# Optimization experiments

Measured on AMD Instinct MI355X. Metric: run time of the kernel, lower is better.

## Reference

```python
import jax, jax.numpy as jnp
import numpy as np

DIM = 64        # feature size per vector
CODES = 512     # codebook size (called d_model in the torch module)
DECAY = 0.99
EPS = 1e-5


def setup_inputs() -> dict:
    key = jax.random.key(0)
    k1, k2 = jax.random.split(key)
    x = jax.random.normal(k1, (64, 64, 64, 64), dtype=jnp.float32)
    embedding = jax.random.normal(k2, (DIM, CODES), dtype=jnp.float32)
    N = jnp.zeros((CODES,), dtype=jnp.float32)
    M = embedding.copy()  # torch module initializes M as embedding.clone()
    return {"x": x, "embedding": embedding, "N": N, "M": M}


def reference(x, embedding, N, M):
    # flatten tokens: [T, DIM]
    flatten = x.reshape(-1, DIM)
    # squared L2 distance to every code: [T, CODES]
    distance = (jnp.sum(flatten * flatten, axis=1, keepdims=True)
                - 2.0 * flatten @ embedding
                + jnp.sum(embedding * embedding, axis=0, keepdims=True))
    max_index = jnp.argmin(distance, axis=1)          # (-distance).max(1) == argmin
    indices = max_index.reshape(x.shape[:-1])
    # gather codes: embedding.T is [CODES, DIM]
    quantize = jnp.take(embedding.T, max_index, axis=0).reshape(x.shape)

    # EMA codebook update (training=True). Avoid materializing onehot:
    # ni = onehot.sum(0); eofx = flatten.T @ onehot  -> segment sums over codes.
    ni = jax.ops.segment_sum(jnp.ones_like(max_index, dtype=jnp.float32),
                             max_index, num_segments=CODES)          # [CODES]
    eofx = jax.ops.segment_sum(flatten, max_index, num_segments=CODES).T  # [DIM, CODES]
    N_new = N * DECAY + (1.0 - DECAY) * ni
    M_new = M * DECAY + (1.0 - DECAY) * eofx
    n = jnp.sum(N_new)
    N_smoothed = (N_new + EPS) / (n + CODES * EPS) * n
    embedding_new = M_new / N_smoothed

    quant_loss = jnp.mean((jax.lax.stop_gradient(x) - quantize) ** 2)
    commitment_loss = jnp.mean((jax.lax.stop_gradient(quantize) - x) ** 2)
    quantize_st = x + jax.lax.stop_gradient(quantize - x)  # straight-through
    return (quantize_st, quant_loss, indices, commitment_loss,
            embedding_new, N_new, M_new)
```

## Files before the change

### kernel.cpp

```cpp
#include <hip/hip_runtime.h>
#include <hip/hip_bf16.h>
#include <math.h>

#define DIM 64
#define CODES 512
#define TOKENS 262144
#define XELEMS 16777216

#define DECAYF 0.99f
#define OMDECAY 0.01f
#define EPSF 1e-5f

#define WS_CNORM 0
#define WS_NI    512
#define WS_EOFX  1024
#define WS_LOSS  33792
#define WS_ET    33808
#define WS_IMG   66576
#define WS_PART  99344
#define PART_STRIDE 33280
#define NPART 512

#define OFF_Q    0
#define OFF_QL   16777216
#define OFF_IDX  16777217
#define OFF_CL   17039361
#define OFF_ENEW 17039362
#define OFF_NNEW 17072130
#define OFF_MNEW 17072642

typedef __attribute__((ext_vector_type(8))) short bf16x8;
typedef __attribute__((ext_vector_type(4))) float f32x4;

static __device__ inline void split_bf(float v, short& hi, short& lo) {
  unsigned int b = __float_as_uint(v);
  unsigned int hb = b & 0xffff0000u;
  float lof = v - __uint_as_float(hb);
  hi = (short)(b >> 16);
  lo = (short)(__float_as_uint(lof) >> 16);
}

__global__ __launch_bounds__(256) void vq_prep(const float* __restrict__ emb,
                                               float* __restrict__ ws) {
  int c = blockIdx.x * 256 + threadIdx.x;
  unsigned short* img = (unsigned short*)(ws + WS_IMG);
  float* eT = ws + WS_ET;
  int cc = c >> 4;
  int n = c & 15;
  float cn = 0.f;
#pragma unroll
  for (int d0 = 0; d0 < DIM; d0 += 4) {
    float v[4];
#pragma unroll
    for (int u = 0; u < 4; ++u) {
      v[u] = emb[(d0 + u) * CODES + c];
      cn = fmaf(v[u], v[u], cn);
    }
    *(float4*)(eT + (size_t)c * DIM + d0) = make_float4(v[0], v[1], v[2], v[3]);
    int kh = d0 >> 5, kk = d0 & 31, qd = kk >> 3, j0 = kk & 7;
    int lane = qd * 16 + n;
    short hi[4], lo[4];
#pragma unroll
    for (int u = 0; u < 4; ++u) split_bf(v[u], hi[u], lo[u]);
    int base = cc * 2048 + kh * 1024 + lane * 8 + j0;
    *(ushort4*)(img + base) =
        make_ushort4((unsigned short)hi[0], (unsigned short)hi[1],
                     (unsigned short)hi[2], (unsigned short)hi[3]);
    *(ushort4*)(img + base + 512) =
        make_ushort4((unsigned short)lo[0], (unsigned short)lo[1],
                     (unsigned short)lo[2], (unsigned short)lo[3]);
  }
  ws[WS_CNORM + c] = cn;
}

__global__ __launch_bounds__(512, 4) void vq_fused(
    const float* __restrict__ x, const float* __restrict__ ws,
    float* __restrict__ loss_sum, float* __restrict__ q_out,
    float* __restrict__ idx_out, float* __restrict__ part_base, int aflush,
    float* __restrict__ ws_acc) {
  __shared__ __align__(16) unsigned char smem[71808];
  float* lds_e = (float*)smem;
  float* lds_n = (float*)(smem + 65664);
  float* cn_l = (float*)(smem + 67712);
  int* win_l = (int*)(smem + 69760);

  const float* eT = ws + WS_ET;
  const unsigned short* gimg = (const unsigned short*)(ws + WS_IMG);

  {
    float4 z = make_float4(0.f, 0.f, 0.f, 0.f);
    float4* zp = (float4*)smem;
    for (int i = threadIdx.x; i < 67712 / 16; i += 512) zp[i] = z;
    for (int i = threadIdx.x; i < CODES; i += 512) cn_l[i] = ws[WS_CNORM + i];
  }
  __syncthreads();

  const int lane = threadIdx.x & 63;
  const int wave = threadIdx.x >> 6;
  const int n = lane & 15;
  const int quad = lane >> 4;
  const int t0 = blockIdx.x * 512 + wave * 64;

  const float INITP = __uint_as_float((__float_as_uint(1e30f) & 0xFFFFFE00u) | 511u);
  float loss = 0.f;

#pragma unroll 1
  for (int pair = 0; pair < 2; ++pair) {
    bf16x8 ah[2][2], al[2][2];
#pragma unroll
    for (int tile = 0; tile < 2; ++tile) {
      const float* xr =
          x + (size_t)(t0 + (pair * 2 + tile) * 16 + n) * DIM + quad * 8;
#pragma unroll
      for (int kh = 0; kh < 2; ++kh) {
        float4 va = *(const float4*)(xr + kh * 32);
        float4 vb = *(const float4*)(xr + kh * 32 + 4);
        float f[8] = {va.x, va.y, va.z, va.w, vb.x, vb.y, vb.z, vb.w};
#pragma unroll
        for (int j = 0; j < 8; ++j) {
          short hi, lo;
          split_bf(-2.f * f[j], hi, lo);
          ah[tile][kh][j] = hi;
          al[tile][kh][j] = lo;
        }
      }
    }

    float v1[2][4], v2[2][4];
#pragma unroll
    for (int tile = 0; tile < 2; ++tile)
#pragma unroll
      for (int r = 0; r < 4; ++r) {
        v1[tile][r] = INITP;
        v2[tile][r] = INITP;
      }

    bf16x8 Pa0, Pa1, Pa2, Pa3, Pb0, Pb1, Pb2, Pb3;
    {
      const unsigned short* bq = gimg + lane * 8;
      Pa0 = *(const bf16x8*)(bq);
      Pa1 = *(const bf16x8*)(bq + 512);
      Pa2 = *(const bf16x8*)(bq + 1024);
      Pa3 = *(const bf16x8*)(bq + 1536);
    }

    auto ccbody = [&](int cc, const bf16x8& ch0, const bf16x8& cl0,
                      const bf16x8& ch1, const bf16x8& cl1, bf16x8& nh0,
                      bf16x8& nl0, bf16x8& nh1, bf16x8& nl1) {
      const unsigned short* bq = gimg + ((cc + 1) & 31) * 2048 + lane * 8;
      nh0 = *(const bf16x8*)(bq);
      nl0 = *(const bf16x8*)(bq + 512);
      nh1 = *(const bf16x8*)(bq + 1024);
      nl1 = *(const bf16x8*)(bq + 1536);
      float cnv = cn_l[cc * 16 + n];
      unsigned int cid = (unsigned int)(cc * 16 + n);
#pragma unroll
      for (int tile = 0; tile < 2; ++tile) {
        f32x4 acc = {0.f, 0.f, 0.f, 0.f};
        acc = __builtin_amdgcn_mfma_f32_16x16x32_bf16(ah[tile][0], ch0, acc, 0, 0, 0);
        acc = __builtin_amdgcn_mfma_f32_16x16x32_bf16(al[tile][0], ch0, acc, 0, 0, 0);
        acc = __builtin_amdgcn_mfma_f32_16x16x32_bf16(ah[tile][0], cl0, acc, 0, 0, 0);
        acc = __builtin_amdgcn_mfma_f32_16x16x32_bf16(ah[tile][1], ch1, acc, 0, 0, 0);
        acc = __builtin_amdgcn_mfma_f32_16x16x32_bf16(al[tile][1], ch1, acc, 0, 0, 0);
        acc = __builtin_amdgcn_mfma_f32_16x16x32_bf16(ah[tile][1], cl1, acc, 0, 0, 0);
#pragma unroll
        for (int r = 0; r < 4; ++r) {
          float s = acc[r] + cnv;
          float sp = __uint_as_float((__float_as_uint(s) & 0xFFFFFE00u) | cid);
          float o1 = v1[tile][r];
          v2[tile][r] = __builtin_amdgcn_fmed3f(sp, o1, v2[tile][r]);
          v1[tile][r] = fminf(sp, o1);
        }
      }
    };

    for (int cc = 0; cc < 32; cc += 2) {
      ccbody(cc, Pa0, Pa1, Pa2, Pa3, Pb0, Pb1, Pb2, Pb3);
      ccbody(cc + 1, Pb0, Pb1, Pb2, Pb3, Pa0, Pa1, Pa2, Pa3);
    }

#pragma unroll
    for (int m = 1; m < 16; m <<= 1) {
#pragma unroll
      for (int tile = 0; tile < 2; ++tile)
#pragma unroll
        for (int r = 0; r < 4; ++r) {
          float o1 = __shfl_xor(v1[tile][r], m, 16);
          float o2 = __shfl_xor(v2[tile][r], m, 16);
          float a = v1[tile][r];
          v1[tile][r] = fminf(a, o1);
          v2[tile][r] = fminf(fminf(v2[tile][r], o2), fmaxf(a, o1));
        }
    }

#pragma unroll
    for (int tile = 0; tile < 2; ++tile) {
      int tt = pair * 2 + tile;
#pragma unroll
      for (int r = 0; r < 4; ++r) {
        int t = t0 + tt * 16 + quad * 4 + r;
        int c1 = (int)(__float_as_uint(v1[tile][r]) & 511u);
        int c2 = (int)(__float_as_uint(v2[tile][r]) & 511u);
        float4 xv = *(const float4*)(x + (size_t)t * DIM + n * 4);
        float4 e1 = *(const float4*)(eT + (size_t)c1 * DIM + n * 4);
        float4 e2 = *(const float4*)(eT + (size_t)c2 * DIM + n * 4);
        float p1 = xv.x * e1.x;
        p1 = fmaf(xv.y, e1.y, p1);
        p1 = fmaf(xv.z, e1.z, p1);
        p1 = fmaf(xv.w, e1.w, p1);
        float p2 = xv.x * e2.x;
        p2 = fmaf(xv.y, e2.y, p2);
        p2 = fmaf(xv.z, e2.z, p2);
        p2 = fmaf(xv.w, e2.w, p2);
#pragma unroll
        for (int m = 1; m < 16; m <<= 1) {
          p1 += __shfl_xor(p1, m, 16);
          p2 += __shfl_xor(p2, m, 16);
        }
        float d1 = fmaf(-2.f, p1, cn_l[c1]);
        float d2 = fmaf(-2.f, p2, cn_l[c2]);
        bool take2 = (d2 < d1) || (d2 == d1 && c2 < c1);
        int w = take2 ? c2 : c1;
        float4 q = take2 ? e2 : e1;
        *(float4*)(q_out + (size_t)t * DIM + n * 4) = q;
        float u0 = xv.x - q.x, u1 = xv.y - q.y;
        float u2 = xv.z - q.z, u3 = xv.w - q.w;
        loss = fmaf(u0, u0, loss);
        loss = fmaf(u1, u1, loss);
        loss = fmaf(u2, u2, loss);
        loss = fmaf(u3, u3, loss);
        if (n == 0) {
          idx_out[t] = (float)w;
          win_l[wave * 64 + tt * 16 + quad * 4 + r] = w;
        }
      }
    }
  }

#pragma unroll
  for (int off = 32; off > 0; off >>= 1) loss += __shfl_down(loss, off, 64);
  if (lane == 0) atomicAdd(loss_sum, loss);

  __syncthreads();

#pragma unroll 1
  for (int kh = 0; kh < 2; ++kh) {
#pragma unroll
    for (int tile = 0; tile < 4; ++tile) {
      int wbi = win_l[wave * 64 + tile * 16 + n];
      if (kh == 0 && quad == 0) atomicAdd(&lds_n[wbi], 1.0f);
      const float* xr =
          x + (size_t)(t0 + tile * 16 + n) * DIM + kh * 32 + quad * 8;
      float4 xa = *(const float4*)(xr);
      float4 xb = *(const float4*)(xr + 4);
      int k0 = quad * 8;
      atomicAdd(&lds_e[(k0 + 0) * 513 + wbi], xa.x);
      atomicAdd(&lds_e[(k0 + 1) * 513 + wbi], xa.y);
      atomicAdd(&lds_e[(k0 + 2) * 513 + wbi], xa.z);
      atomicAdd(&lds_e[(k0 + 3) * 513 + wbi], xa.w);
      atomicAdd(&lds_e[(k0 + 4) * 513 + wbi], xb.x);
      atomicAdd(&lds_e[(k0 + 5) * 513 + wbi], xb.y);
      atomicAdd(&lds_e[(k0 + 6) * 513 + wbi], xb.z);
      atomicAdd(&lds_e[(k0 + 7) * 513 + wbi], xb.w);
    }
    __syncthreads();
    if (aflush) {
      if (kh == 0) {
        for (int i = threadIdx.x; i < CODES; i += 512) {
          float v = lds_n[i];
          if (v != 0.f) atomicAdd(&ws_acc[WS_NI + i], v);
        }
      }
      for (int i = threadIdx.x; i < 32 * CODES; i += 512) {
        int k = i >> 9, c = i & 511;
        float v = lds_e[k * 513 + c];
        if (v != 0.f) atomicAdd(&ws_acc[WS_EOFX + kh * 32 * CODES + i], v);
        if (kh == 0) lds_e[k * 513 + c] = 0.f;
      }
    } else {
      float* dest = part_base + (size_t)blockIdx.x * PART_STRIDE;
      if (kh == 0) {
        for (int i = threadIdx.x; i < CODES; i += 512) dest[i] = lds_n[i];
      }
      for (int i = threadIdx.x; i < 32 * CODES; i += 512) {
        int k = i >> 9, c = i & 511;
        dest[CODES + kh * 32 * CODES + i] = lds_e[k * 513 + c];
        if (kh == 0) lds_e[k * 513 + c] = 0.f;
      }
    }
    if (kh == 0) __syncthreads();
  }
}

__global__ __launch_bounds__(256) void vq_reduce(const float* __restrict__ part,
                                                 float* __restrict__ ws, int P) {
  int i = blockIdx.x * 256 + threadIdx.x;
  if (i >= PART_STRIDE) return;
  float a0 = 0.f, a1 = 0.f, a2 = 0.f, a3 = 0.f;
  int p = 0;
  for (; p + 3 < P; p += 4) {
    a0 += part[(size_t)(p + 0) * PART_STRIDE + i];
    a1 += part[(size_t)(p + 1) * PART_STRIDE + i];
    a2 += part[(size_t)(p + 2) * PART_STRIDE + i];
    a3 += part[(size_t)(p + 3) * PART_STRIDE + i];
  }
  for (; p < P; ++p) a0 += part[(size_t)p * PART_STRIDE + i];
  ws[WS_NI + i] = (a0 + a1) + (a2 + a3);
}

__global__ __launch_bounds__(512) void vq_final(const float* __restrict__ Nin,
                                                const float* __restrict__ Min,
                                                const float* __restrict__ ws,
                                                float* __restrict__ out) {
  __shared__ float red[512];
  int c = threadIdx.x;
  int d = blockIdx.x;
  float niv = ws[WS_NI + c];
  float Nn = Nin[c] * DECAYF + OMDECAY * niv;
  red[c] = Nn;
  __syncthreads();
#pragma unroll
  for (int s = 256; s > 0; s >>= 1) {
    if (c < s) red[c] += red[c + s];
    __syncthreads();
  }
  float nsum = red[0];
  float Nsm = (Nn + EPSF) / (nsum + (float)CODES * EPSF) * nsum;
  float m = Min[d * CODES + c] * DECAYF + OMDECAY * ws[WS_EOFX + d * CODES + c];
  out[OFF_MNEW + d * CODES + c] = m;
  out[OFF_ENEW + d * CODES + c] = m / Nsm;
  if (d == 0) {
    out[OFF_NNEW + c] = Nn;
    if (c == 0) {
      float l = ws[WS_LOSS] / (float)XELEMS;
      out[OFF_QL] = l;
      out[OFF_CL] = l;
    }
  }
}

extern "C" void kernel_launch(void* const* d_in, const int* in_sizes, int n_in,
                              void* d_out, int out_size, void* d_ws, size_t ws_size,
                              hipStream_t stream) {
  const float* x = (const float*)d_in[0];
  const float* emb = (const float*)d_in[1];
  const float* Nin = (const float*)d_in[2];
  const float* Min = (const float*)d_in[3];
  float* out = (float*)d_out;
  float* ws = (float*)d_ws;

  size_t avail = ws_size / 4;
  int aflush = (avail < (size_t)WS_PART + (size_t)NPART * PART_STRIDE) ? 1 : 0;

  hipMemsetAsync(ws + WS_NI, 0, (size_t)(WS_ET - WS_NI) * sizeof(float), stream);

  vq_prep<<<2, 256, 0, stream>>>(emb, ws);

  vq_fused<<<TOKENS / 512, 512, 0, stream>>>(
      x, ws, ws + WS_LOSS, out + OFF_Q, out + OFF_IDX, ws + WS_PART, aflush, ws);

  if (!aflush) {
    vq_reduce<<<(PART_STRIDE + 255) / 256, 256, 0, stream>>>(ws + WS_PART, ws,
                                                             NPART);
  }

  vq_final<<<DIM, 512, 0, stream>>>(Nin, Min, ws, out);
}
```

Before: 350.2 us.

## Stage codebook tiles through LDS with async triple buffering; split reduce across partitions

Codebook image chunks are no longer loaded per wave straight from global memory into registers. Wave 0 now streams them into a triple-buffered LDS ring with global_load_lds, gated by explicit vmcnt waits and workgroup barriers, so the other waves read them from LDS. This cuts redundant global and L2 traffic for the code images, at the cost of one barrier per code chunk. The LDS zeroing moves after the distance loop because the ring reuses that memory, and vq_reduce is split over 8 partition groups that combine results with atomic adds to expose more parallelism.

New measurement: 311.6 us. 1.12x faster.

```diff
diff --git a/kernel.cpp b/kernel.cpp
--- a/kernel.cpp
+++ b/kernel.cpp
@@ -31,6 +31,11 @@
 
 typedef __attribute__((ext_vector_type(8))) short bf16x8;
 typedef __attribute__((ext_vector_type(4))) float f32x4;
+
+#define GLOAD_LDS16(gp, lp)                                        \
+  __builtin_amdgcn_global_load_lds(                                \
+      (const __attribute__((address_space(1))) void*)(gp),         \
+      (__attribute__((address_space(3))) void*)(lp), 16, 0, 0)
 
 static __device__ inline void split_bf(float v, short& hi, short& lo) {
   unsigned int b = __float_as_uint(v);
@@ -85,15 +90,9 @@
   int* win_l = (int*)(smem + 69760);
 
   const float* eT = ws + WS_ET;
-  const unsigned short* gimg = (const unsigned short*)(ws + WS_IMG);
-
-  {
-    float4 z = make_float4(0.f, 0.f, 0.f, 0.f);
-    float4* zp = (float4*)smem;
-    for (int i = threadIdx.x; i < 67712 / 16; i += 512) zp[i] = z;
-    for (int i = threadIdx.x; i < CODES; i += 512) cn_l[i] = ws[WS_CNORM + i];
-  }
-  __syncthreads();
+  const char* gib = (const char*)(ws + WS_IMG);
+
+  for (int i = threadIdx.x; i < CODES; i += 512) cn_l[i] = ws[WS_CNORM + i];
 
   const int lane = threadIdx.x & 63;
   const int wave = threadIdx.x >> 6;
@@ -135,34 +134,41 @@
         v2[tile][r] = INITP;
       }
 
-    bf16x8 Pa0, Pa1, Pa2, Pa3, Pb0, Pb1, Pb2, Pb3;
-    {
-      const unsigned short* bq = gimg + lane * 8;
-      Pa0 = *(const bf16x8*)(bq);
-      Pa1 = *(const bf16x8*)(bq + 512);
-      Pa2 = *(const bf16x8*)(bq + 1024);
-      Pa3 = *(const bf16x8*)(bq + 1536);
-    }
-
-    auto ccbody = [&](int cc, const bf16x8& ch0, const bf16x8& cl0,
-                      const bf16x8& ch1, const bf16x8& cl1, bf16x8& nh0,
-                      bf16x8& nl0, bf16x8& nh1, bf16x8& nl1) {
-      const unsigned short* bq = gimg + ((cc + 1) & 31) * 2048 + lane * 8;
-      nh0 = *(const bf16x8*)(bq);
-      nl0 = *(const bf16x8*)(bq + 512);
-      nh1 = *(const bf16x8*)(bq + 1024);
-      nl1 = *(const bf16x8*)(bq + 1536);
+    if (wave == 0) {
+#pragma unroll
+      for (int c0 = 0; c0 < 2; ++c0)
+#pragma unroll
+        for (int q = 0; q < 4; ++q)
+          GLOAD_LDS16(gib + c0 * 4096 + q * 1024 + (size_t)lane * 16,
+                      (char*)smem + c0 * 4096 + q * 1024);
+    }
+    __syncthreads();
+
+#pragma unroll 1
+    for (int cc = 0; cc < 32; ++cc) {
+      const unsigned short* bp =
+          (const unsigned short*)((const char*)smem + (cc % 3) * 4096);
+      bf16x8 bh0 = *(const bf16x8*)(bp + lane * 8);
+      bf16x8 bl0 = *(const bf16x8*)(bp + 512 + lane * 8);
+      bf16x8 bh1 = *(const bf16x8*)(bp + 1024 + lane * 8);
+      bf16x8 bl1 = *(const bf16x8*)(bp + 1536 + lane * 8);
+      if (wave == 0 && cc < 30) {
+        char* lb = (char*)smem + ((cc + 2) % 3) * 4096;
+        const char* gs = gib + (cc + 2) * 4096 + (size_t)lane * 16;
+#pragma unroll
+        for (int q = 0; q < 4; ++q) GLOAD_LDS16(gs + q * 1024, lb + q * 1024);
+      }
       float cnv = cn_l[cc * 16 + n];
       unsigned int cid = (unsigned int)(cc * 16 + n);
 #pragma unroll
       for (int tile = 0; tile < 2; ++tile) {
         f32x4 acc = {0.f, 0.f, 0.f, 0.f};
-        acc = __builtin_amdgcn_mfma_f32_16x16x32_bf16(ah[tile][0], ch0, acc, 0, 0, 0);
-        acc = __builtin_amdgcn_mfma_f32_16x16x32_bf16(al[tile][0], ch0, acc, 0, 0, 0);
-        acc = __builtin_amdgcn_mfma_f32_16x16x32_bf16(ah[tile][0], cl0, acc, 0, 0, 0);
-        acc = __builtin_amdgcn_mfma_f32_16x16x32_bf16(ah[tile][1], ch1, acc, 0, 0, 0);
-        acc = __builtin_amdgcn_mfma_f32_16x16x32_bf16(al[tile][1], ch1, acc, 0, 0, 0);
-        acc = __builtin_amdgcn_mfma_f32_16x16x32_bf16(ah[tile][1], cl1, acc, 0, 0, 0);
+        acc = __builtin_amdgcn_mfma_f32_16x16x32_bf16(ah[tile][0], bh0, acc, 0, 0, 0);
+        acc = __builtin_amdgcn_mfma_f32_16x16x32_bf16(al[tile][0], bh0, acc, 0, 0, 0);
+        acc = __builtin_amdgcn_mfma_f32_16x16x32_bf16(ah[tile][0], bl0, acc, 0, 0, 0);
+        acc = __builtin_amdgcn_mfma_f32_16x16x32_bf16(ah[tile][1], bh1, acc, 0, 0, 0);
+        acc = __builtin_amdgcn_mfma_f32_16x16x32_bf16(al[tile][1], bh1, acc, 0, 0, 0);
+        acc = __builtin_amdgcn_mfma_f32_16x16x32_bf16(ah[tile][1], bl1, acc, 0, 0, 0);
 #pragma unroll
         for (int r = 0; r < 4; ++r) {
           float s = acc[r] + cnv;
@@ -172,11 +178,14 @@
           v1[tile][r] = fminf(sp, o1);
         }
       }
-    };
-
-    for (int cc = 0; cc < 32; cc += 2) {
-      ccbody(cc, Pa0, Pa1, Pa2, Pa3, Pb0, Pb1, Pb2, Pb3);
-      ccbody(cc + 1, Pb0, Pb1, Pb2, Pb3, Pa0, Pa1, Pa2, Pa3);
+      if (cc < 30) {
+        asm volatile("s_waitcnt vmcnt(4)" ::: "memory");
+      } else {
+        asm volatile("s_waitcnt vmcnt(0)" ::: "memory");
+      }
+      __builtin_amdgcn_sched_barrier(0);
+      __builtin_amdgcn_s_barrier();
+      __builtin_amdgcn_sched_barrier(0);
     }
 
 #pragma unroll
@@ -241,6 +250,12 @@
   for (int off = 32; off > 0; off >>= 1) loss += __shfl_down(loss, off, 64);
   if (lane == 0) atomicAdd(loss_sum, loss);
 
+  __syncthreads();
+  {
+    float4 z = make_float4(0.f, 0.f, 0.f, 0.f);
+    float4* zp = (float4*)smem;
+    for (int i = threadIdx.x; i < 67712 / 16; i += 512) zp[i] = z;
+  }
   __syncthreads();
 
 #pragma unroll 1
@@ -296,16 +311,19 @@
                                                  float* __restrict__ ws, int P) {
   int i = blockIdx.x * 256 + threadIdx.x;
   if (i >= PART_STRIDE) return;
+  int cp = P >> 3;
+  int p0 = blockIdx.y * cp;
+  int pe = p0 + cp;
   float a0 = 0.f, a1 = 0.f, a2 = 0.f, a3 = 0.f;
-  int p = 0;
-  for (; p + 3 < P; p += 4) {
+  int p = p0;
+  for (; p + 3 < pe; p += 4) {
     a0 += part[(size_t)(p + 0) * PART_STRIDE + i];
     a1 += part[(size_t)(p + 1) * PART_STRIDE + i];
     a2 += part[(size_t)(p + 2) * PART_STRIDE + i];
     a3 += part[(size_t)(p + 3) * PART_STRIDE + i];
   }
-  for (; p < P; ++p) a0 += part[(size_t)p * PART_STRIDE + i];
-  ws[WS_NI + i] = (a0 + a1) + (a2 + a3);
+  for (; p < pe; ++p) a0 += part[(size_t)p * PART_STRIDE + i];
+  atomicAdd(&ws[WS_NI + i], (a0 + a1) + (a2 + a3));
 }
 
 __global__ __launch_bounds__(512) void vq_final(const float* __restrict__ Nin,
@@ -360,8 +378,8 @@
       x, ws, ws + WS_LOSS, out + OFF_Q, out + OFF_IDX, ws + WS_PART, aflush, ws);
 
   if (!aflush) {
-    vq_reduce<<<(PART_STRIDE + 255) / 256, 256, 0, stream>>>(ws + WS_PART, ws,
-                                                             NPART);
+    vq_reduce<<<dim3((PART_STRIDE + 255) / 256, 8), 256, 0, stream>>>(
+        ws + WS_PART, ws, NPART);
   }
 
   vq_final<<<DIM, 512, 0, stream>>>(Nin, Min, ws, out);
```

## Split fused VQ kernel into screening and scatter kernels; parallelize partial reduce

Applied to the files above, without the earlier changes.

Splits the fused distance/argmin and segment-sum kernel into two. The screening kernel uses 256-thread blocks and only a small LDS footprint, which should raise occupancy for the compute-heavy phase. A separate scatter kernel rereads x and the indices to build the per-block partial sums in LDS. The reduce kernel now splits the partials across 8 y-blocks and combines them with atomics, which relies on the NI/EOFX region being zeroed by the memset. The cost is a second full read of x and the indices, plus an extra kernel launch.

After: 327.4 us. 1.07x faster.

```diff
diff --git a/kernel.cpp b/kernel.cpp
--- a/kernel.cpp
+++ b/kernel.cpp
@@ -73,33 +73,23 @@
   ws[WS_CNORM + c] = cn;
 }
 
-__global__ __launch_bounds__(512, 4) void vq_fused(
+__global__ __launch_bounds__(256, 4) void vq_screen(
     const float* __restrict__ x, const float* __restrict__ ws,
     float* __restrict__ loss_sum, float* __restrict__ q_out,
-    float* __restrict__ idx_out, float* __restrict__ part_base, int aflush,
-    float* __restrict__ ws_acc) {
-  __shared__ __align__(16) unsigned char smem[71808];
-  float* lds_e = (float*)smem;
-  float* lds_n = (float*)(smem + 65664);
-  float* cn_l = (float*)(smem + 67712);
-  int* win_l = (int*)(smem + 69760);
+    float* __restrict__ idx_out) {
+  __shared__ float cn_l[CODES];
 
   const float* eT = ws + WS_ET;
   const unsigned short* gimg = (const unsigned short*)(ws + WS_IMG);
 
-  {
-    float4 z = make_float4(0.f, 0.f, 0.f, 0.f);
-    float4* zp = (float4*)smem;
-    for (int i = threadIdx.x; i < 67712 / 16; i += 512) zp[i] = z;
-    for (int i = threadIdx.x; i < CODES; i += 512) cn_l[i] = ws[WS_CNORM + i];
-  }
+  for (int i = threadIdx.x; i < CODES; i += 256) cn_l[i] = ws[WS_CNORM + i];
   __syncthreads();
 
   const int lane = threadIdx.x & 63;
   const int wave = threadIdx.x >> 6;
   const int n = lane & 15;
   const int quad = lane >> 4;
-  const int t0 = blockIdx.x * 512 + wave * 64;
+  const int t0 = blockIdx.x * 256 + wave * 64;
 
   const float INITP = __uint_as_float((__float_as_uint(1e30f) & 0xFFFFFE00u) | 511u);
   float loss = 0.f;
@@ -229,10 +219,7 @@
         loss = fmaf(u1, u1, loss);
         loss = fmaf(u2, u2, loss);
         loss = fmaf(u3, u3, loss);
-        if (n == 0) {
-          idx_out[t] = (float)w;
-          win_l[wave * 64 + tt * 16 + quad * 4 + r] = w;
-        }
+        if (n == 0) idx_out[t] = (float)w;
       }
     }
   }
@@ -240,7 +227,29 @@
 #pragma unroll
   for (int off = 32; off > 0; off >>= 1) loss += __shfl_down(loss, off, 64);
   if (lane == 0) atomicAdd(loss_sum, loss);
-
+}
+
+__global__ __launch_bounds__(512, 2) void vq_scatter(
+    const float* __restrict__ x, const float* __restrict__ idx_out,
+    float* __restrict__ part_base, int aflush, float* __restrict__ ws_acc) {
+  __shared__ __align__(16) unsigned char smem[69760];
+  float* lds_e = (float*)smem;
+  float* lds_n = (float*)(smem + 65664);
+  int* win_l = (int*)(smem + 67712);
+
+  const int lane = threadIdx.x & 63;
+  const int wave = threadIdx.x >> 6;
+  const int n = lane & 15;
+  const int quad = lane >> 4;
+  const int t0 = blockIdx.x * 512 + wave * 64;
+
+  {
+    float4 z = make_float4(0.f, 0.f, 0.f, 0.f);
+    float4* zp = (float4*)smem;
+    for (int i = threadIdx.x; i < 67712 / 16; i += 512) zp[i] = z;
+  }
+  if (threadIdx.x < 512)
+    win_l[threadIdx.x] = (int)idx_out[blockIdx.x * 512 + threadIdx.x];
   __syncthreads();
 
 #pragma unroll 1
@@ -296,16 +305,19 @@
                                                  float* __restrict__ ws, int P) {
   int i = blockIdx.x * 256 + threadIdx.x;
   if (i >= PART_STRIDE) return;
+  int cp = P >> 3;
+  int p0 = blockIdx.y * cp;
+  int pe = p0 + cp;
   float a0 = 0.f, a1 = 0.f, a2 = 0.f, a3 = 0.f;
-  int p = 0;
-  for (; p + 3 < P; p += 4) {
+  int p = p0;
+  for (; p + 3 < pe; p += 4) {
     a0 += part[(size_t)(p + 0) * PART_STRIDE + i];
     a1 += part[(size_t)(p + 1) * PART_STRIDE + i];
     a2 += part[(size_t)(p + 2) * PART_STRIDE + i];
     a3 += part[(size_t)(p + 3) * PART_STRIDE + i];
   }
-  for (; p < P; ++p) a0 += part[(size_t)p * PART_STRIDE + i];
-  ws[WS_NI + i] = (a0 + a1) + (a2 + a3);
+  for (; p < pe; ++p) a0 += part[(size_t)p * PART_STRIDE + i];
+  atomicAdd(&ws[WS_NI + i], (a0 + a1) + (a2 + a3));
 }
 
 __global__ __launch_bounds__(512) void vq_final(const float* __restrict__ Nin,
@@ -356,12 +368,15 @@
 
   vq_prep<<<2, 256, 0, stream>>>(emb, ws);
 
-  vq_fused<<<TOKENS / 512, 512, 0, stream>>>(
-      x, ws, ws + WS_LOSS, out + OFF_Q, out + OFF_IDX, ws + WS_PART, aflush, ws);
+  vq_screen<<<TOKENS / 256, 256, 0, stream>>>(x, ws, ws + WS_LOSS, out + OFF_Q,
+                                              out + OFF_IDX);
+
+  vq_scatter<<<TOKENS / 512, 512, 0, stream>>>(x, out + OFF_IDX, ws + WS_PART,
+                                               aflush, ws);
 
   if (!aflush) {
-    vq_reduce<<<(PART_STRIDE + 255) / 256, 256, 0, stream>>>(ws + WS_PART, ws,
-                                                             NPART);
+    vq_reduce<<<dim3((PART_STRIDE + 255) / 256, 8), 256, 0, stream>>>(
+        ws + WS_PART, ws, NPART);
   }
 
   vq_final<<<DIM, 512, 0, stream>>>(Nin, Min, ws, out);
```
